# Optimization experiments

Hardware: AMD Instinct MI355X
Metric: run time of the kernel (lower is better)

The kernel has to match this reference:

```python
import jax, jax.numpy as jnp
import numpy as np

N, IN, OUT, T = 500000, 128, 64, 8

def setup_inputs() -> dict:
    key = jax.random.key(0)
    k1, k2, k3, k4 = jax.random.split(key, 4)
    x = jax.random.normal(k1, (N, IN), dtype=jnp.float32)
    node_type = jax.random.randint(k2, (N,), 0, T, dtype=jnp.int32)
    # per-type Linear weights, stored as [T, IN, OUT] so x @ W[t] matches torch Linear
    W = jax.random.normal(k3, (T, IN, OUT), dtype=jnp.float32) * (1.0 / np.sqrt(IN))
    b = jax.random.normal(k4, (T, OUT), dtype=jnp.float32) * 0.01
    return {"x": x, "node_type": node_type, "W": W, "b": b}

def reference(x, node_type, W, b):
    # emb_x[mask_t] = x[mask_t] @ W[t] + b[t], for each node type t.
    # Vectorized: loop over the small fixed number of types, masked accumulate.
    T_ = W.shape[0]
    out = jnp.zeros((x.shape[0], W.shape[2]), dtype=x.dtype)
    for t in range(T_):
        y_t = x @ W[t] + b[t]                      # [N, OUT]
        mask = (node_type == t)[:, None]           # [N, 1]
        out = jnp.where(mask, y_t, out)
    return out
```

## Files before the change

### kernel.cpp

```cpp
#include <hip/hip_runtime.h>
#include <hip/hip_bf16.h>

#define NT   8
#define INF  128
#define OUTF 64

typedef __attribute__((ext_vector_type(8))) short short8;
typedef __attribute__((ext_vector_type(4))) float f32x4;

__device__ __forceinline__ short f2bf(float f) {
  __hip_bfloat16 h = __float2bfloat16(f);
  return __builtin_bit_cast(short, h);
}

__global__ void hl_wconv(const float* __restrict__ W, short* __restrict__ wbf) {
  const int tid   = blockIdx.x * blockDim.x + threadIdx.x;
  const int combo = tid >> 6;
  const int lane  = tid & 63;
  const int t = combo >> 4, s = (combo >> 2) & 3, nb = combo & 3;
  const int q = lane >> 4, c = lane & 15;
  const float* Wt = W + t * INF * OUTF;
  short8 v;
  #pragma unroll
  for (int j = 0; j < 8; ++j)
    v[j] = f2bf(Wt[(s * 32 + q * 8 + j) * OUTF + nb * 16 + c]);
  *(short8*)(wbf + (size_t)tid * 8) = v;
}

__global__ __launch_bounds__(256) void hl_main(
    const float* __restrict__ x, const int* __restrict__ nty,
    const short* __restrict__ wbf, const float* __restrict__ b,
    float* __restrict__ out, int N) {
  const int ntiles = (N + 15) >> 4;
  const int wave = threadIdx.x >> 6;
  const int lane = threadIdx.x & 63;
  const int q = lane >> 4, c = lane & 15;
  const int nwaves = gridDim.x * 4;
  const short* wp = wbf + (size_t)lane * 8;

  for (int tile = blockIdx.x * 4 + wave; tile < ntiles; tile += nwaves) {
    const int base = tile * 16;
    int rowa = base + c; if (rowa > N - 1) rowa = N - 1;
    const int ty = nty[rowa];
    const float* xr = x + (size_t)rowa * INF;

    short8 A[4];
    #pragma unroll
    for (int s = 0; s < 4; ++s) {
      f32x4 v0 = *(const f32x4*)(xr + s * 32 + q * 8);
      f32x4 v1 = *(const f32x4*)(xr + s * 32 + q * 8 + 4);
      short8 a;
      #pragma unroll
      for (int j = 0; j < 4; ++j) { a[j] = f2bf(v0[j]); a[j + 4] = f2bf(v1[j]); }
      A[s] = a;
    }

    f32x4 acc[4] = {{0,0,0,0},{0,0,0,0},{0,0,0,0},{0,0,0,0}};
    const short8 z8 = {0,0,0,0,0,0,0,0};

    short8 BA[4], BB[4];
    #pragma unroll
    for (int nb = 0; nb < 4; ++nb) BA[nb] = *(const short8*)(wp + (size_t)nb * 512);

    #pragma unroll 1
    for (int t = 0; t < NT; ++t) {
      const int f0 = t * 16;
      const int fn = (f0 + 16 < 128) ? f0 + 16 : 124;
      #pragma unroll
      for (int nb = 0; nb < 4; ++nb) BB[nb] = *(const short8*)(wp + (size_t)(f0 + 4 + nb) * 512);
      { short8 am = (ty == t) ? A[0] : z8;
        #pragma unroll
        for (int nb = 0; nb < 4; ++nb)
          acc[nb] = __builtin_amdgcn_mfma_f32_16x16x32_bf16(am, BA[nb], acc[nb], 0, 0, 0); }
      #pragma unroll
      for (int nb = 0; nb < 4; ++nb) BA[nb] = *(const short8*)(wp + (size_t)(f0 + 8 + nb) * 512);
      { short8 am = (ty == t) ? A[1] : z8;
        #pragma unroll
        for (int nb = 0; nb < 4; ++nb)
          acc[nb] = __builtin_amdgcn_mfma_f32_16x16x32_bf16(am, BB[nb], acc[nb], 0, 0, 0); }
      #pragma unroll
      for (int nb = 0; nb < 4; ++nb) BB[nb] = *(const short8*)(wp + (size_t)(f0 + 12 + nb) * 512);
      { short8 am = (ty == t) ? A[2] : z8;
        #pragma unroll
        for (int nb = 0; nb < 4; ++nb)
          acc[nb] = __builtin_amdgcn_mfma_f32_16x16x32_bf16(am, BA[nb], acc[nb], 0, 0, 0); }
      #pragma unroll
      for (int nb = 0; nb < 4; ++nb) BA[nb] = *(const short8*)(wp + (size_t)(fn + nb) * 512);
      { short8 am = (ty == t) ? A[3] : z8;
        #pragma unroll
        for (int nb = 0; nb < 4; ++nb)
          acc[nb] = __builtin_amdgcn_mfma_f32_16x16x32_bf16(am, BB[nb], acc[nb], 0, 0, 0); }
    }

    const int rbase = base + q * 4;
    int4 tyv;
    if (rbase + 3 < N) {
      tyv = *(const int4*)(nty + rbase);
    } else {
      int t0 = rbase + 0 < N ? nty[rbase + 0] : 0;
      int t1 = rbase + 1 < N ? nty[rbase + 1] : 0;
      int t2 = rbase + 2 < N ? nty[rbase + 2] : 0;
      int t3 = rbase + 3 < N ? nty[rbase + 3] : 0;
      tyv.x = t0; tyv.y = t1; tyv.z = t2; tyv.w = t3;
    }
    const int trs[4] = {tyv.x, tyv.y, tyv.z, tyv.w};
    #pragma unroll
    for (int r = 0; r < 4; ++r) {
      const int row = rbase + r;
      if (row < N) {
        const float* br = b + trs[r] * OUTF + c;
        float* orow = out + (size_t)row * OUTF + c;
        #pragma unroll
        for (int nb = 0; nb < 4; ++nb)
          orow[nb * 16] = acc[nb][r] + br[nb * 16];
      }
    }
  }
}

extern "C" void kernel_launch(void* const* d_in, const int* in_sizes, int n_in,
                              void* d_out, int out_size, void* d_ws, size_t ws_size,
                              hipStream_t stream) {
  const float* x  = (const float*)d_in[0];
  const int*   nt = (const int*)d_in[1];
  const float* W  = (const float*)d_in[2];
  const float* b  = (const float*)d_in[3];
  float* out = (float*)d_out;
  const int N = in_sizes[1];
  short* wbf = (short*)d_ws;

  hl_wconv<<<32, 256, 0, stream>>>(W, wbf);
  hl_main<<<2048, 256, 0, stream>>>(x, nt, wbf, b, out, N);
}
```

Measured before the change: 479.6 us.

## Process four row tiles per wave to reuse weight fragments across MFMAs

Each wave now handles 64 rows as four 16-row tiles, loading each bf16 weight fragment once and applying it to all four tiles' masked MFMAs. This cuts the per-row weight fetch traffic from L2/cache by a factor of four. It raises register usage for A fragments and accumulators, sets launch bounds to 2 blocks, and shrinks the grid to 512 blocks, which may reduce latency hiding.

```diff
diff --git a/kernel.cpp b/kernel.cpp
--- a/kernel.cpp
+++ b/kernel.cpp
@@ -4,6 +4,7 @@
 #define NT   8
 #define INF  128
 #define OUTF 64
+#define MT   4
 
 typedef __attribute__((ext_vector_type(8))) short short8;
 typedef __attribute__((ext_vector_type(4))) float f32x4;
@@ -27,36 +28,46 @@
   *(short8*)(wbf + (size_t)tid * 8) = v;
 }
 
-__global__ __launch_bounds__(256) void hl_main(
+__global__ __launch_bounds__(256, 2) void hl_main(
     const float* __restrict__ x, const int* __restrict__ nty,
     const short* __restrict__ wbf, const float* __restrict__ b,
     float* __restrict__ out, int N) {
-  const int ntiles = (N + 15) >> 4;
+  const int npass = (N + 63) >> 6;
   const int wave = threadIdx.x >> 6;
   const int lane = threadIdx.x & 63;
   const int q = lane >> 4, c = lane & 15;
   const int nwaves = gridDim.x * 4;
   const short* wp = wbf + (size_t)lane * 8;
 
-  for (int tile = blockIdx.x * 4 + wave; tile < ntiles; tile += nwaves) {
-    const int base = tile * 16;
-    int rowa = base + c; if (rowa > N - 1) rowa = N - 1;
-    const int ty = nty[rowa];
-    const float* xr = x + (size_t)rowa * INF;
+  for (int pass = blockIdx.x * 4 + wave; pass < npass; pass += nwaves) {
+    const int base = pass * 64;
 
-    short8 A[4];
+    short8 A[MT][4];
+    int tys[MT];
     #pragma unroll
-    for (int s = 0; s < 4; ++s) {
-      f32x4 v0 = *(const f32x4*)(xr + s * 32 + q * 8);
-      f32x4 v1 = *(const f32x4*)(xr + s * 32 + q * 8 + 4);
-      short8 a;
+    for (int i = 0; i < MT; ++i) {
+      int rowa = base + i * 16 + c;
+      if (rowa > N - 1) rowa = N - 1;
+      tys[i] = nty[rowa];
+      const float* xr = x + (size_t)rowa * INF;
       #pragma unroll
-      for (int j = 0; j < 4; ++j) { a[j] = f2bf(v0[j]); a[j + 4] = f2bf(v1[j]); }
-      A[s] = a;
+      for (int s = 0; s < 4; ++s) {
+        f32x4 v0 = *(const f32x4*)(xr + s * 32 + q * 8);
+        f32x4 v1 = *(const f32x4*)(xr + s * 32 + q * 8 + 4);
+        short8 a;
+        #pragma unroll
+        for (int j = 0; j < 4; ++j) { a[j] = f2bf(v0[j]); a[j + 4] = f2bf(v1[j]); }
+        A[i][s] = a;
+      }
     }
 
-    f32x4 acc[4] = {{0,0,0,0},{0,0,0,0},{0,0,0,0},{0,0,0,0}};
-    const short8 z8 = {0,0,0,0,0,0,0,0};
+    f32x4 acc[MT][4];
+    #pragma unroll
+    for (int i = 0; i < MT; ++i)
+      #pragma unroll
+      for (int nb = 0; nb < 4; ++nb) acc[i][nb] = (f32x4){0, 0, 0, 0};
+
+    const short8 z8 = {0, 0, 0, 0, 0, 0, 0, 0};
 
     short8 BA[4], BB[4];
     #pragma unroll
@@ -64,55 +75,60 @@
 
     #pragma unroll 1
     for (int t = 0; t < NT; ++t) {
-      const int f0 = t * 16;
-      const int fn = (f0 + 16 < 128) ? f0 + 16 : 124;
       #pragma unroll
-      for (int nb = 0; nb < 4; ++nb) BB[nb] = *(const short8*)(wp + (size_t)(f0 + 4 + nb) * 512);
-      { short8 am = (ty == t) ? A[0] : z8;
-        #pragma unroll
-        for (int nb = 0; nb < 4; ++nb)
-          acc[nb] = __builtin_amdgcn_mfma_f32_16x16x32_bf16(am, BA[nb], acc[nb], 0, 0, 0); }
-      #pragma unroll
-      for (int nb = 0; nb < 4; ++nb) BA[nb] = *(const short8*)(wp + (size_t)(f0 + 8 + nb) * 512);
-      { short8 am = (ty == t) ? A[1] : z8;
-        #pragma unroll
-        for (int nb = 0; nb < 4; ++nb)
-          acc[nb] = __builtin_amdgcn_mfma_f32_16x16x32_bf16(am, BB[nb], acc[nb], 0, 0, 0); }
-      #pragma unroll
-      for (int nb = 0; nb < 4; ++nb) BB[nb] = *(const short8*)(wp + (size_t)(f0 + 12 + nb) * 512);
-      { short8 am = (ty == t) ? A[2] : z8;
-        #pragma unroll
-        for (int nb = 0; nb < 4; ++nb)
-          acc[nb] = __builtin_amdgcn_mfma_f32_16x16x32_bf16(am, BA[nb], acc[nb], 0, 0, 0); }
-      #pragma unroll
-      for (int nb = 0; nb < 4; ++nb) BA[nb] = *(const short8*)(wp + (size_t)(fn + nb) * 512);
-      { short8 am = (ty == t) ? A[3] : z8;
-        #pragma unroll
-        for (int nb = 0; nb < 4; ++nb)
-          acc[nb] = __builtin_amdgcn_mfma_f32_16x16x32_bf16(am, BB[nb], acc[nb], 0, 0, 0); }
+      for (int s = 0; s < 4; ++s) {
+        const int g = t * 4 + s;
+        const int gn = (g + 1 < 32) ? g + 1 : 31;
+        if ((s & 1) == 0) {
+          #pragma unroll
+          for (int nb = 0; nb < 4; ++nb)
+            BB[nb] = *(const short8*)(wp + (size_t)(gn * 4 + nb) * 512);
+          #pragma unroll
+          for (int i = 0; i < MT; ++i) {
+            short8 am = (tys[i] == t) ? A[i][s] : z8;
+            #pragma unroll
+            for (int nb = 0; nb < 4; ++nb)
+              acc[i][nb] = __builtin_amdgcn_mfma_f32_16x16x32_bf16(am, BA[nb], acc[i][nb], 0, 0, 0);
+          }
+        } else {
+          #pragma unroll
+          for (int nb = 0; nb < 4; ++nb)
+            BA[nb] = *(const short8*)(wp + (size_t)(gn * 4 + nb) * 512);
+          #pragma unroll
+          for (int i = 0; i < MT; ++i) {
+            short8 am = (tys[i] == t) ? A[i][s] : z8;
+            #pragma unroll
+            for (int nb = 0; nb < 4; ++nb)
+              acc[i][nb] = __builtin_amdgcn_mfma_f32_16x16x32_bf16(am, BB[nb], acc[i][nb], 0, 0, 0);
+          }
+        }
+      }
     }
 
-    const int rbase = base + q * 4;
-    int4 tyv;
-    if (rbase + 3 < N) {
-      tyv = *(const int4*)(nty + rbase);
-    } else {
-      int t0 = rbase + 0 < N ? nty[rbase + 0] : 0;
-      int t1 = rbase + 1 < N ? nty[rbase + 1] : 0;
-      int t2 = rbase + 2 < N ? nty[rbase + 2] : 0;
-      int t3 = rbase + 3 < N ? nty[rbase + 3] : 0;
-      tyv.x = t0; tyv.y = t1; tyv.z = t2; tyv.w = t3;
-    }
-    const int trs[4] = {tyv.x, tyv.y, tyv.z, tyv.w};
     #pragma unroll
-    for (int r = 0; r < 4; ++r) {
-      const int row = rbase + r;
-      if (row < N) {
-        const float* br = b + trs[r] * OUTF + c;
-        float* orow = out + (size_t)row * OUTF + c;
-        #pragma unroll
-        for (int nb = 0; nb < 4; ++nb)
-          orow[nb * 16] = acc[nb][r] + br[nb * 16];
+    for (int i = 0; i < MT; ++i) {
+      const int rbase = base + i * 16 + q * 4;
+      if (rbase >= N) continue;
+      int4 tyv;
+      if (rbase + 3 < N) {
+        tyv = *(const int4*)(nty + rbase);
+      } else {
+        tyv.x = rbase + 0 < N ? nty[rbase + 0] : 0;
+        tyv.y = rbase + 1 < N ? nty[rbase + 1] : 0;
+        tyv.z = rbase + 2 < N ? nty[rbase + 2] : 0;
+        tyv.w = rbase + 3 < N ? nty[rbase + 3] : 0;
+      }
+      const int trs[4] = {tyv.x, tyv.y, tyv.z, tyv.w};
+      #pragma unroll
+      for (int r = 0; r < 4; ++r) {
+        const int row = rbase + r;
+        if (row < N) {
+          const float* br = b + trs[r] * OUTF + c;
+          float* orow = out + (size_t)row * OUTF + c;
+          #pragma unroll
+          for (int nb = 0; nb < 4; ++nb)
+            orow[nb * 16] = acc[i][nb][r] + br[nb * 16];
+        }
       }
     }
   }
@@ -130,5 +146,5 @@
   short* wbf = (short*)d_ws;
 
   hl_wconv<<<32, 256, 0, stream>>>(W, wbf);
-  hl_main<<<2048, 256, 0, stream>>>(x, nt, wbf, b, out, N);
+  hl_main<<<512, 256, 0, stream>>>(x, nt, wbf, b, out, N);
 }
```

Result: faster. 428.7 us (-10.6%).
